# Kernel optimization log

Measured on AMD Instinct MI355X. Metric: run time of the kernel, lower is better.

The kernel has to match this reference:

```python
import jax, jax.numpy as jnp
import numpy as np

B, L, D = 4, 1024, 768
H, Dh = 12, 64
W_ONE_SIDED = 512


def setup_inputs() -> dict:
    key = jax.random.key(0)
    ks = jax.random.split(key, 14)
    std = 0.02
    def lin(k):
        return jax.random.normal(k, (D, D), jnp.float32) * std
    inp = {
        "hidden_states": jax.random.normal(ks[0], (B, L, D), jnp.float32),
        "Wq": lin(ks[1]), "bq": jnp.zeros((D,), jnp.float32),
        "Wk": lin(ks[2]), "bk": jnp.zeros((D,), jnp.float32),
        "Wv": lin(ks[3]), "bv": jnp.zeros((D,), jnp.float32),
        "Wqg": lin(ks[4]), "bqg": jnp.zeros((D,), jnp.float32),
        "Wkg": lin(ks[5]), "bkg": jnp.zeros((D,), jnp.float32),
        "Wvg": lin(ks[6]), "bvg": jnp.zeros((D,), jnp.float32),
    }
    pos = jnp.arange(L)
    # last 64 positions padded; first 8 tokens are global (CLS-like)
    inp["is_index_masked"] = jnp.broadcast_to(pos >= L - 64, (B, L))
    inp["is_index_global_attn"] = jnp.broadcast_to(pos < 8, (B, L))
    return inp


def _split_heads(x):
    # [B, L, D] -> [B, L, H, Dh]
    return x.reshape(B, L, H, Dh)


def reference(hidden_states, Wq, bq, Wk, bk, Wv, bv, Wqg, bqg, Wkg, bkg, Wvg, bvg,
              is_index_masked, is_index_global_attn):
    scale = 1.0 / np.sqrt(Dh)
    x = hidden_states
    Ql = _split_heads(x @ Wq + bq)
    Kl = _split_heads(x @ Wk + bk)
    Vl = _split_heads(x @ Wv + bv)
    Qg = _split_heads(x @ Wqg + bqg)
    Kg = _split_heads(x @ Wkg + bkg)
    Vg = _split_heads(x @ Wvg + bvg)

    neg_inf = jnp.finfo(x.dtype).min
    not_masked = ~is_index_masked
    not_global = ~is_index_global_attn

    # ---- local branch: doubled-K scores [B,H,L,2L] (first half: global-key
    # columns, second half: banded local-key columns), joint softmax ----
    s = jnp.einsum('bqhd,bkhd->bhqk', Ql, Kl) * scale  # [B,H,L,L]
    idx = jnp.arange(L)
    band = jnp.abs(idx[None, :] - idx[:, None]) <= W_ONE_SIDED  # [L,L]
    global_valid = (is_index_global_attn & not_masked)[:, None, None, :]      # [B,1,1,L]
    local_valid = (band[None, :, :] & (not_masked & not_global)[:, None, :])[:, None, :, :]  # [B,1,L,L]
    s_first = jnp.where(global_valid, s, neg_inf)
    s_second = jnp.where(local_valid, s, neg_inf)
    scores_local = jnp.concatenate([s_first, s_second], axis=-1)  # [B,H,L,2L]
    probs = jax.nn.softmax(scores_local.astype(jnp.float32), axis=-1).astype(x.dtype)
    probs = jnp.where(is_index_masked[:, None, :, None], 0.0, probs)
    # (p1 + p2) @ V  ==  p1 @ V + p2 @ V  since K/V are duplicated
    p_sum = probs[..., :L] + probs[..., L:]
    attn_local = jnp.einsum('bhqk,bkhd->bqhd', p_sum, Vl).reshape(B, L, D)

    # ---- global branch: full attention over global projections ----
    sg = jnp.einsum('bqhd,bkhd->bhqk', Qg, Kg) * scale
    sg = jnp.where(is_index_masked[:, None, None, :], neg_inf, sg)
    pg = jax.nn.softmax(sg.astype(jnp.float32), axis=-1).astype(x.dtype)
    pg = jnp.where(is_index_masked[:, None, :, None], 0.0, pg)
    attn_global = jnp.einsum('bhqk,bkhd->bqhd', pg, Vg).reshape(B, L, D)

    # ---- gated combine: global tokens take the global-attention output ----
    output = jnp.where(is_index_global_attn[:, :, None], attn_global, attn_local)
    return output
```

## Files before the change

### kernel.cpp

```cpp
#include <hip/hip_runtime.h>
#include <stdint.h>
#include <math.h>

#define LSEQ 1024
#define NB 4
#define DM 768
#define NHEAD 12
#define HD 64
#define LVALID 960
#define WIN 512

typedef unsigned short u16;
typedef __attribute__((ext_vector_type(8))) short s16x8;
typedef __attribute__((ext_vector_type(4))) float f32x4;

__device__ __forceinline__ u16 f2bf(float f) {
  union { float f; uint32_t u; } v; v.f = f;
  uint32_t r = v.u + 0x7fffu + ((v.u >> 16) & 1u);
  return (u16)(r >> 16);
}
__device__ __forceinline__ float bf2f(u16 h) {
  union { uint32_t u; float f; } v; v.u = ((uint32_t)h) << 16;
  return v.f;
}
__device__ __forceinline__ int swz8(int row, int chunk) {
  return row * 8 + (chunk ^ (row & 7));
}

__device__ __forceinline__ void gload_lds16(const void* g, void* l) {
  __builtin_amdgcn_global_load_lds(
      (const __attribute__((address_space(1))) unsigned int*)g,
      (__attribute__((address_space(3))) unsigned int*)l, 16, 0, 0);
}

#define BARW()                                  \
  do {                                          \
    asm volatile("" ::: "memory");              \
    __builtin_amdgcn_s_barrier();               \
    asm volatile("" ::: "memory");              \
  } while (0)
#define LGKM0() asm volatile("s_waitcnt lgkmcnt(0)" ::: "memory")
#define VMC4() asm volatile("s_waitcnt vmcnt(4)" ::: "memory")
#define VMC0() asm volatile("s_waitcnt vmcnt(0)" ::: "memory")

struct WPtrs { const float* w[6]; };
struct GemmPtrs { const u16* wt[6]; const float* bias[6]; u16* out[6]; };

__global__ __launch_bounds__(256) void prep(const float* __restrict__ x, u16* __restrict__ xb,
                                            WPtrs P, u16* __restrict__ wtb) {
  int bi = blockIdx.x;
  if (bi >= 864) {
    int i = ((bi - 864) * 256 + threadIdx.x) * 8;
    float4 a = *(const float4*)(x + i);
    float4 bq = *(const float4*)(x + i + 4);
    u16 t[8];
    t[0] = f2bf(a.x); t[1] = f2bf(a.y); t[2] = f2bf(a.z); t[3] = f2bf(a.w);
    t[4] = f2bf(bq.x); t[5] = f2bf(bq.y); t[6] = f2bf(bq.z); t[7] = f2bf(bq.w);
    *(uint4*)(xb + i) = *(uint4*)t;
    return;
  }
  int mat = bi / 144, rem = bi - mat * 144;
  int gx = rem % 12, gy = rem / 12;
  const float* W = P.w[mat];
  u16* Wt = wtb + (size_t)mat * DM * DM;
  __shared__ u16 tile[64][72];
  int k0 = gx * 64, n0 = gy * 64;
  int r4 = threadIdx.x >> 4;
  int c4 = (threadIdx.x & 15) * 4;
#pragma unroll
  for (int it = 0; it < 4; it++) {
    int r = it * 16 + r4;
    float4 v = *(const float4*)(W + (size_t)(k0 + r) * DM + n0 + c4);
    tile[c4 + 0][r] = f2bf(v.x);
    tile[c4 + 1][r] = f2bf(v.y);
    tile[c4 + 2][r] = f2bf(v.z);
    tile[c4 + 3][r] = f2bf(v.w);
  }
  __syncthreads();
  int rw = threadIdx.x >> 3, cw = (threadIdx.x & 7) * 8;
#pragma unroll
  for (int it = 0; it < 2; it++) {
    int r = it * 32 + rw;
    *(uint4*)(Wt + (size_t)(n0 + r) * DM + k0 + cw) = *(uint4*)&tile[r][cw];
  }
}

__global__ __launch_bounds__(512, 2) void gemm6(const u16* __restrict__ Xb, GemmPtrs P,
                                                u16* __restrict__ Vt) {
  int mat = blockIdx.z;
  int m0 = blockIdx.x * 256, n0 = blockIdx.y * 256;
  if (mat == 3 && (m0 & 1023) != 0) return;
  __shared__ __align__(16) u16 SMEM[65536];
  const u16* Wt = P.wt[mat];
  int tid = threadIdx.x;
  int w = tid >> 6, lane = tid & 63, qd = lane >> 4, l16 = lane & 15;
  int wm = w >> 2, wn = w & 3;
  int cx = l16 & 7;

  f32x4 acc[8][4];
  const f32x4 fz = {0.f, 0.f, 0.f, 0.f};
#pragma unroll
  for (int i = 0; i < 8; i++)
#pragma unroll
    for (int j = 0; j < 4; j++) acc[i][j] = fz;

  int aoff[2][2], boff[2][2];
#pragma unroll
  for (int j = 0; j < 2; j++) {
    int s = j * 512 + tid;
    int row = s >> 3;
    int col = ((s & 7) ^ (row & 7)) * 8;
#pragma unroll
    for (int h = 0; h < 2; h++) {
      aoff[j][h] = (m0 + h * 128 + row) * DM + col;
      boff[j][h] = (n0 + h * 128 + row) * DM + col;
    }
  }

  auto stageA = [&](int t, int h) {
#pragma unroll
    for (int j = 0; j < 2; j++)
      gload_lds16(Xb + (size_t)aoff[j][h] + t * 64,
                  &SMEM[(t & 1) * 32768 + h * 8192 + (j * 512 + w * 64) * 8]);
  };
  auto stageB = [&](int t, int h) {
#pragma unroll
    for (int j = 0; j < 2; j++)
      gload_lds16(Wt + (size_t)boff[j][h] + t * 64,
                  &SMEM[(t & 1) * 32768 + 16384 + h * 8192 + (j * 512 + w * 64) * 8]);
  };

  stageA(0, 0); stageA(0, 1);
  stageB(0, 0); stageB(0, 1);
  stageB(1, 0); stageB(1, 1);
  VMC4();
  BARW();

  const int rB = (wn & 1) * 64 + l16;

  auto tile = [&](int u) {
    const int buf = u & 1;
    const u16* Ab = &SMEM[buf * 32768 + wm * 8192];
    const u16* Bb = &SMEM[buf * 32768 + 16384 + (wn >> 1) * 8192];
    s16x8 af[4][2], bfr[4][2];
#pragma unroll
    for (int mi = 0; mi < 4; mi++)
#pragma unroll
      for (int ks = 0; ks < 2; ks++)
        af[mi][ks] = *(const s16x8*)(Ab + (mi * 16 + l16) * 64 + ((ks * 4 + qd) ^ cx) * 8);
#pragma unroll
    for (int ni = 0; ni < 2; ni++)
#pragma unroll
      for (int ks = 0; ks < 2; ks++)
        bfr[ni][ks] = *(const s16x8*)(Bb + (rB + ni * 16) * 64 + ((ks * 4 + qd) ^ cx) * 8);
    if (u < 11) stageA(u + 1, 0);
    BARW();
    LGKM0();
    __builtin_amdgcn_s_setprio(1);
#pragma unroll
    for (int mi = 0; mi < 4; mi++)
#pragma unroll
      for (int ni = 0; ni < 2; ni++)
#pragma unroll
        for (int ks = 0; ks < 2; ks++)
          acc[mi][ni] = __builtin_amdgcn_mfma_f32_16x16x32_bf16(af[mi][ks], bfr[ni][ks],
                                                                acc[mi][ni], 0, 0, 0);
    __builtin_amdgcn_s_setprio(0);
    BARW();
#pragma unroll
    for (int ni = 2; ni < 4; ni++)
#pragma unroll
      for (int ks = 0; ks < 2; ks++)
        bfr[ni][ks] = *(const s16x8*)(Bb + (rB + ni * 16) * 64 + ((ks * 4 + qd) ^ cx) * 8);
    if (u < 11) stageA(u + 1, 1);
    BARW();
    LGKM0();
    __builtin_amdgcn_s_setprio(1);
#pragma unroll
    for (int mi = 0; mi < 4; mi++)
#pragma unroll
      for (int ni = 2; ni < 4; ni++)
#pragma unroll
        for (int ks = 0; ks < 2; ks++)
          acc[mi][ni] = __builtin_amdgcn_mfma_f32_16x16x32_bf16(af[mi][ks], bfr[ni][ks],
                                                                acc[mi][ni], 0, 0, 0);
    __builtin_amdgcn_s_setprio(0);
    BARW();
#pragma unroll
    for (int mi = 0; mi < 4; mi++)
#pragma unroll
      for (int ks = 0; ks < 2; ks++)
        af[mi][ks] = *(const s16x8*)(Ab + ((mi + 4) * 16 + l16) * 64 + ((ks * 4 + qd) ^ cx) * 8);
    if (u < 10) stageB(u + 2, 0);
    BARW();
    LGKM0();
    __builtin_amdgcn_s_setprio(1);
#pragma unroll
    for (int mi = 0; mi < 4; mi++)
#pragma unroll
      for (int ni = 0; ni < 2; ni++)
#pragma unroll
        for (int ks = 0; ks < 2; ks++)
          acc[mi + 4][ni] = __builtin_amdgcn_mfma_f32_16x16x32_bf16(af[mi][ks], bfr[ni][ks],
                                                                    acc[mi + 4][ni], 0, 0, 0);
    __builtin_amdgcn_s_setprio(0);
    BARW();
    if (u < 10) {
      stageB(u + 2, 1);
      VMC4();
    } else {
      VMC0();
    }
    BARW();
    __builtin_amdgcn_s_setprio(1);
#pragma unroll
    for (int mi = 0; mi < 4; mi++)
#pragma unroll
      for (int ni = 2; ni < 4; ni++)
#pragma unroll
        for (int ks = 0; ks < 2; ks++)
          acc[mi + 4][ni] = __builtin_amdgcn_mfma_f32_16x16x32_bf16(af[mi][ks], bfr[ni][ks],
                                                                    acc[mi + 4][ni], 0, 0, 0);
    __builtin_amdgcn_s_setprio(0);
    BARW();
  };

  for (int u = 0; u < 12; ++u) tile(u);

  const float* bias = P.bias[mat];
  u16* outp = P.out[mat];
  int bb = m0 >> 10, t0 = m0 & 1023;
  __syncthreads();
  u16* Cs = &SMEM[0];
#pragma unroll
  for (int ni = 0; ni < 4; ni++) {
    int n = wn * 64 + ni * 16 + l16;
    float bvl = bias[n0 + n];
#pragma unroll
    for (int mi = 0; mi < 8; mi++) {
      int mb = wm * 128 + mi * 16 + qd * 4;
      u16 pk[4];
#pragma unroll
      for (int r = 0; r < 4; r++) {
        u16 v = f2bf(acc[mi][ni][r] + bvl);
        Cs[(mb + r) * 256 + n] = v;
        pk[r] = v;
      }
      if (mat == 2) {
        int gn = n0 + n, hh = gn >> 6, dd = gn & 63;
        *(uint2*)(Vt + ((size_t)(bb * NHEAD + hh) * HD + dd) * LSEQ + t0 + mb) =
            *(uint2*)pk;
      }
    }
  }
  __syncthreads();
#pragma unroll
  for (int it = 0; it < 16; it++) {
    int c = it * 512 + tid;
    int row = c >> 5, col = c & 31;
    *(uint4*)(outp + (size_t)(m0 + row) * DM + n0 + col * 8) = ((const uint4*)Cs)[c];
  }
}

__global__ __launch_bounds__(128) void attn_local(
    const u16* __restrict__ Qb, const u16* __restrict__ Kb,
    const u16* __restrict__ Vt, float* __restrict__ out) {
  int q0 = blockIdx.x * 32, h = blockIdx.y, b = blockIdx.z;
  __shared__ u16 Ks[64 * 64], Vs[64 * 64];
  __shared__ u16 Ps[2][16 * 64];
  int tid = threadIdx.x, w = tid >> 6, lane = tid & 63, qd = lane >> 4, l16 = lane & 15;

  int rowK[4], colK[4];
#pragma unroll
  for (int i = 0; i < 4; i++) {
    int s = (w * 4 + i) * 64 + lane;
    rowK[i] = s >> 3;
    colK[i] = ((s & 7) ^ (rowK[i] & 7)) * 8;
  }

  const u16* qrow = Qb + (size_t)(b * LSEQ + q0 + w * 16 + l16) * DM + h * HD;
  s16x8 af0 = *(const s16x8*)(qrow + qd * 8);
  s16x8 af1 = *(const s16x8*)(qrow + 32 + qd * 8);

  float l_part[4] = {0.f, 0.f, 0.f, 0.f};
  f32x4 aO[4];
  const f32x4 fz = {0.f, 0.f, 0.f, 0.f};
#pragma unroll
  for (int nt = 0; nt < 4; nt++) aO[nt] = fz;

  for (int c = 0; c < 16; c++) {
    int kb = c * 64;
    if (c > 0 && !(kb < LVALID && kb + 63 >= q0 - WIN && kb <= q0 + 31 + WIN)) continue;
    __syncthreads();
#pragma unroll
    for (int i = 0; i < 4; i++) {
      gload_lds16(Kb + (size_t)(b * LSEQ + kb + rowK[i]) * DM + h * HD + colK[i],
                  Ks + (size_t)(w * 4 + i) * 512);
      gload_lds16(Vt + (size_t)((b * NHEAD + h) * HD + rowK[i]) * LSEQ + kb + colK[i],
                  Vs + (size_t)(w * 4 + i) * 512);
    }
    __syncthreads();

    float p[4][4];
#pragma unroll
    for (int nt = 0; nt < 4; nt++) {
      s16x8 bk0 = *(const s16x8*)(Ks + swz8(nt * 16 + l16, qd) * 8);
      s16x8 bk1 = *(const s16x8*)(Ks + swz8(nt * 16 + l16, 4 + qd) * 8);
      f32x4 s = fz;
      s = __builtin_amdgcn_mfma_f32_16x16x32_bf16(af0, bk0, s, 0, 0, 0);
      s = __builtin_amdgcn_mfma_f32_16x16x32_bf16(af1, bk1, s, 0, 0, 0);
      int k = kb + nt * 16 + l16;
#pragma unroll
      for (int r = 0; r < 4; r++) {
        int q = q0 + w * 16 + qd * 4 + r;
        bool valid = (k < 8) || (k < LVALID && (k - q) <= WIN && (q - k) <= WIN);
        float sv = valid ? s[r] * 0.125f : -1e30f;
        p[nt][r] = __expf(sv);
        l_part[r] += p[nt][r];
      }
    }

#pragma unroll
    for (int nt = 0; nt < 4; nt++) {
      int chunk = nt * 2 + (l16 >> 3);
      int within = l16 & 7;
#pragma unroll
      for (int r = 0; r < 4; r++) {
        int qrow2 = qd * 4 + r;
        Ps[w][swz8(qrow2, chunk) * 8 + within] = f2bf(p[nt][r]);
      }
    }

    s16x8 pf0 = *(const s16x8*)(&Ps[w][0] + swz8(l16, qd) * 8);
    s16x8 pf1 = *(const s16x8*)(&Ps[w][0] + swz8(l16, 4 + qd) * 8);
#pragma unroll
    for (int nt = 0; nt < 4; nt++) {
      s16x8 v0 = *(const s16x8*)(Vs + swz8(nt * 16 + l16, qd) * 8);
      s16x8 v1 = *(const s16x8*)(Vs + swz8(nt * 16 + l16, 4 + qd) * 8);
      aO[nt] = __builtin_amdgcn_mfma_f32_16x16x32_bf16(pf0, v0, aO[nt], 0, 0, 0);
      aO[nt] = __builtin_amdgcn_mfma_f32_16x16x32_bf16(pf1, v1, aO[nt], 0, 0, 0);
    }
  }

#pragma unroll
  for (int off = 1; off < 16; off <<= 1)
#pragma unroll
    for (int r = 0; r < 4; r++) l_part[r] += __shfl_xor(l_part[r], off);
  float inv[4];
#pragma unroll
  for (int r = 0; r < 4; r++) inv[r] = 1.0f / l_part[r];
#pragma unroll
  for (int nt = 0; nt < 4; nt++)
#pragma unroll
    for (int r = 0; r < 4; r++) {
      int q = q0 + w * 16 + qd * 4 + r;
      out[(size_t)(b * LSEQ + q) * DM + h * HD + nt * 16 + l16] = aO[nt][r] * inv[r];
    }
}

__global__ __launch_bounds__(256) void attn_global(
    const u16* __restrict__ Qgb, const u16* __restrict__ Kgb,
    const u16* __restrict__ Vgb, float* __restrict__ out) {
  int h = blockIdx.x, b = blockIdx.y;
  __shared__ float p_lds[8][960];
  __shared__ float partial[4][8][64];
  int tid = threadIdx.x, w = tid >> 6, lane = tid & 63, qd = lane >> 4, l16 = lane & 15;

  {
    float4 z = {0.f, 0.f, 0.f, 0.f};
#pragma unroll
    for (int it = 0; it < 4; it++) {
      int idx = it * 256 + tid;
      int r = idx >> 4, cc = idx & 15;
      *(float4*)(out + (size_t)(b * LSEQ + LVALID + r) * DM + h * HD + cc * 4) = z;
    }
  }

  const u16* qbase = Qgb + (size_t)(b * LSEQ + l16) * DM + h * HD;
  s16x8 af0 = *(const s16x8*)(qbase + qd * 8);
  s16x8 af1 = *(const s16x8*)(qbase + 32 + qd * 8);
  const f32x4 fz = {0.f, 0.f, 0.f, 0.f};
#pragma unroll
  for (int t = 0; t < 15; t++) {
    int kb = (w + 4 * t) * 16;
    const u16* kbase = Kgb + (size_t)(b * LSEQ + kb + l16) * DM + h * HD;
    s16x8 bk0 = *(const s16x8*)(kbase + qd * 8);
    s16x8 bk1 = *(const s16x8*)(kbase + 32 + qd * 8);
    f32x4 s = fz;
    s = __builtin_amdgcn_mfma_f32_16x16x32_bf16(af0, bk0, s, 0, 0, 0);
    s = __builtin_amdgcn_mfma_f32_16x16x32_bf16(af1, bk1, s, 0, 0, 0);
    if (qd < 2) {
#pragma unroll
      for (int r = 0; r < 4; r++)
        p_lds[qd * 4 + r][kb + l16] = s[r] * 0.125f;
    }
  }
  __syncthreads();

#pragma unroll
  for (int qi = 0; qi < 2; qi++) {
    int q = w * 2 + qi;
    float m = -1e30f;
#pragma unroll
    for (int ki = 0; ki < 15; ki++) m = fmaxf(m, p_lds[q][ki * 64 + lane]);
#pragma unroll
    for (int off = 1; off < 64; off <<= 1) m = fmaxf(m, __shfl_xor(m, off));
    float e[15], ssum = 0.f;
#pragma unroll
    for (int ki = 0; ki < 15; ki++) {
      e[ki] = __expf(p_lds[q][ki * 64 + lane] - m);
      ssum += e[ki];
    }
#pragma unroll
    for (int off = 1; off < 64; off <<= 1) ssum += __shfl_xor(ssum, off);
    float inv = 1.0f / ssum;
#pragma unroll
    for (int ki = 0; ki < 15; ki++) p_lds[q][ki * 64 + lane] = e[ki] * inv;
  }
  __syncthreads();

  float acc[8] = {0.f, 0.f, 0.f, 0.f, 0.f, 0.f, 0.f, 0.f};
  const u16* vcol = Vgb + (size_t)b * LSEQ * DM + h * HD + lane;
  for (int kg = 0; kg < 60; kg++) {
    int k0 = w * 240 + kg * 4;
    float v0 = bf2f(vcol[(size_t)(k0 + 0) * DM]);
    float v1 = bf2f(vcol[(size_t)(k0 + 1) * DM]);
    float v2 = bf2f(vcol[(size_t)(k0 + 2) * DM]);
    float v3 = bf2f(vcol[(size_t)(k0 + 3) * DM]);
#pragma unroll
    for (int q = 0; q < 8; q++) {
      float4 p4 = *(const float4*)&p_lds[q][k0];
      acc[q] += p4.x * v0 + p4.y * v1 + p4.z * v2 + p4.w * v3;
    }
  }
#pragma unroll
  for (int q = 0; q < 8; q++) partial[w][q][lane] = acc[q];
  __syncthreads();
#pragma unroll
  for (int i = 0; i < 2; i++) {
    int idx = tid + 256 * i;
    int q = idx >> 6, d = idx & 63;
    float sum = partial[0][q][d] + partial[1][q][d] + partial[2][q][d] + partial[3][q][d];
    out[(size_t)(b * LSEQ + q) * DM + h * HD + d] = sum;
  }
}

extern "C" void kernel_launch(void* const* d_in, const int* in_sizes, int n_in,
                              void* d_out, int out_size, void* d_ws, size_t ws_size,
                              hipStream_t stream) {
  const float* x = (const float*)d_in[0];
  float* out = (float*)d_out;
  char* ws = (char*)d_ws;

  const size_t XB_SZ = (size_t)4096 * DM * 2;
  const size_t WT_SZ = (size_t)6 * DM * DM * 2;
  const size_t MAT_SZ = (size_t)4096 * DM;
  u16* Xb = (u16*)ws;
  u16* Wt = (u16*)(ws + XB_SZ);
  u16* QKV = (u16*)(ws + XB_SZ + WT_SZ);
  u16* Vt = (u16*)(ws + XB_SZ + WT_SZ + (size_t)6 * MAT_SZ * 2);

  u16* Ql = QKV + 0 * MAT_SZ;
  u16* Kl = QKV + 1 * MAT_SZ;
  u16* Vl = QKV + 2 * MAT_SZ;
  u16* Qg = QKV + 3 * MAT_SZ;
  u16* Kg = QKV + 4 * MAT_SZ;
  u16* Vg = QKV + 5 * MAT_SZ;

  WPtrs wp;
  wp.w[0] = (const float*)d_in[1];
  wp.w[1] = (const float*)d_in[3];
  wp.w[2] = (const float*)d_in[5];
  wp.w[3] = (const float*)d_in[7];
  wp.w[4] = (const float*)d_in[9];
  wp.w[5] = (const float*)d_in[11];
  prep<<<2400, 256, 0, stream>>>(x, Xb, wp, Wt);

  GemmPtrs gp;
  const int bidx[6] = {2, 4, 6, 8, 10, 12};
  u16* outs[6] = {Ql, Kl, Vl, Qg, Kg, Vg};
  for (int i = 0; i < 6; i++) {
    gp.wt[i] = Wt + (size_t)i * DM * DM;
    gp.bias[i] = (const float*)d_in[bidx[i]];
    gp.out[i] = outs[i];
  }
  gemm6<<<dim3(16, 3, 6), 512, 0, stream>>>(Xb, gp, Vt);

  attn_local<<<dim3(30, 12, 4), 128, 0, stream>>>(Ql, Kl, Vt, out);
  attn_global<<<dim3(12, 4), 256, 0, stream>>>(Qg, Kg, Vg, out);
}
```

Before: 201.2 us.

## Compact gemm grid with XCD-aware mapping, deepen A prefetch, read K/V directly in local attention

The projection GEMM launch drops its early-exiting blocks and maps a 1D grid of 252 blocks onto matrices and tiles so neighbouring work lands on the same XCD. The A-tile prefetch is moved one phase earlier, raising the outstanding-load wait count. Local attention drops its LDS staging of K and V along with both block barriers and loads MFMA operands straight from global memory, relying on the cache. It also remaps blocks so that each XCD handles contiguous (head, batch) groups. The trade-off is more uncoalesced global reads per wave in exchange for removing synchronisation.

```diff
diff --git a/kernel.cpp b/kernel.cpp
--- a/kernel.cpp
+++ b/kernel.cpp
@@ -40,7 +40,7 @@
     asm volatile("" ::: "memory");              \
   } while (0)
 #define LGKM0() asm volatile("s_waitcnt lgkmcnt(0)" ::: "memory")
-#define VMC4() asm volatile("s_waitcnt vmcnt(4)" ::: "memory")
+#define VMC6() asm volatile("s_waitcnt vmcnt(6)" ::: "memory")
 #define VMC0() asm volatile("s_waitcnt vmcnt(0)" ::: "memory")
 
 struct WPtrs { const float* w[6]; };
@@ -87,9 +87,23 @@
 
 __global__ __launch_bounds__(512, 2) void gemm6(const u16* __restrict__ Xb, GemmPtrs P,
                                                 u16* __restrict__ Vt) {
-  int mat = blockIdx.z;
-  int m0 = blockIdx.x * 256, n0 = blockIdx.y * 256;
-  if (mat == 3 && (m0 & 1023) != 0) return;
+  int lid = blockIdx.x;
+  int xcd = lid & 7, pos = lid >> 3;
+  int wid = (xcd < 4) ? xcd * 32 + pos : 128 + (xcd - 4) * 31 + pos;
+  int gid = wid >> 4, m = wid & 15;
+  int mat, x, y;
+  if (gid < 15) {
+    int mm = gid / 3;
+    mat = (mm < 3) ? mm : mm + 1;
+    y = gid - mm * 3;
+    x = m;
+  } else {
+    mat = 3;
+    x = (m / 3) * 4;
+    y = m - (m / 3) * 3;
+  }
+  int m0 = x * 256, n0 = y * 256;
+
   __shared__ __align__(16) u16 SMEM[65536];
   const u16* Wt = P.wt[mat];
   int tid = threadIdx.x;
@@ -133,7 +147,8 @@
   stageA(0, 0); stageA(0, 1);
   stageB(0, 0); stageB(0, 1);
   stageB(1, 0); stageB(1, 1);
-  VMC4();
+  stageA(1, 0);
+  VMC6();
   BARW();
 
   const int rB = (wn & 1) * 64 + l16;
@@ -153,7 +168,7 @@
 #pragma unroll
       for (int ks = 0; ks < 2; ks++)
         bfr[ni][ks] = *(const s16x8*)(Bb + (rB + ni * 16) * 64 + ((ks * 4 + qd) ^ cx) * 8);
-    if (u < 11) stageA(u + 1, 0);
+    if (u <= 10) stageA(u + 1, 1);
     BARW();
     LGKM0();
     __builtin_amdgcn_s_setprio(1);
@@ -172,7 +187,6 @@
 #pragma unroll
       for (int ks = 0; ks < 2; ks++)
         bfr[ni][ks] = *(const s16x8*)(Bb + (rB + ni * 16) * 64 + ((ks * 4 + qd) ^ cx) * 8);
-    if (u < 11) stageA(u + 1, 1);
     BARW();
     LGKM0();
     __builtin_amdgcn_s_setprio(1);
@@ -191,7 +205,7 @@
 #pragma unroll
       for (int ks = 0; ks < 2; ks++)
         af[mi][ks] = *(const s16x8*)(Ab + ((mi + 4) * 16 + l16) * 64 + ((ks * 4 + qd) ^ cx) * 8);
-    if (u < 10) stageB(u + 2, 0);
+    if (u <= 9) stageB(u + 2, 0);
     BARW();
     LGKM0();
     __builtin_amdgcn_s_setprio(1);
@@ -205,9 +219,10 @@
                                                                     acc[mi + 4][ni], 0, 0, 0);
     __builtin_amdgcn_s_setprio(0);
     BARW();
-    if (u < 10) {
+    if (u <= 9) {
       stageB(u + 2, 1);
-      VMC4();
+      stageA(u + 2, 0);
+      VMC6();
     } else {
       VMC0();
     }
@@ -265,23 +280,21 @@
 __global__ __launch_bounds__(128) void attn_local(
     const u16* __restrict__ Qb, const u16* __restrict__ Kb,
     const u16* __restrict__ Vt, float* __restrict__ out) {
-  int q0 = blockIdx.x * 32, h = blockIdx.y, b = blockIdx.z;
-  __shared__ u16 Ks[64 * 64], Vs[64 * 64];
+  int bid = blockIdx.x;
+  int wid = (bid & 7) * 180 + (bid >> 3);
+  int q0 = (wid % 30) * 32;
+  int hb = wid / 30;
+  int h = hb % NHEAD, b = hb / NHEAD;
   __shared__ u16 Ps[2][16 * 64];
   int tid = threadIdx.x, w = tid >> 6, lane = tid & 63, qd = lane >> 4, l16 = lane & 15;
-
-  int rowK[4], colK[4];
-#pragma unroll
-  for (int i = 0; i < 4; i++) {
-    int s = (w * 4 + i) * 64 + lane;
-    rowK[i] = s >> 3;
-    colK[i] = ((s & 7) ^ (rowK[i] & 7)) * 8;
-  }
 
   const u16* qrow = Qb + (size_t)(b * LSEQ + q0 + w * 16 + l16) * DM + h * HD;
   s16x8 af0 = *(const s16x8*)(qrow + qd * 8);
   s16x8 af1 = *(const s16x8*)(qrow + 32 + qd * 8);
 
+  const u16* kb_base = Kb + (size_t)(b * LSEQ) * DM + h * HD;
+  const u16* vt_base = Vt + (size_t)((b * NHEAD + h) * HD) * LSEQ;
+
   float l_part[4] = {0.f, 0.f, 0.f, 0.f};
   f32x4 aO[4];
   const f32x4 fz = {0.f, 0.f, 0.f, 0.f};
@@ -291,21 +304,13 @@
   for (int c = 0; c < 16; c++) {
     int kb = c * 64;
     if (c > 0 && !(kb < LVALID && kb + 63 >= q0 - WIN && kb <= q0 + 31 + WIN)) continue;
-    __syncthreads();
-#pragma unroll
-    for (int i = 0; i < 4; i++) {
-      gload_lds16(Kb + (size_t)(b * LSEQ + kb + rowK[i]) * DM + h * HD + colK[i],
-                  Ks + (size_t)(w * 4 + i) * 512);
-      gload_lds16(Vt + (size_t)((b * NHEAD + h) * HD + rowK[i]) * LSEQ + kb + colK[i],
-                  Vs + (size_t)(w * 4 + i) * 512);
-    }
-    __syncthreads();
 
     float p[4][4];
 #pragma unroll
     for (int nt = 0; nt < 4; nt++) {
-      s16x8 bk0 = *(const s16x8*)(Ks + swz8(nt * 16 + l16, qd) * 8);
-      s16x8 bk1 = *(const s16x8*)(Ks + swz8(nt * 16 + l16, 4 + qd) * 8);
+      const u16* krow = kb_base + (size_t)(kb + nt * 16 + l16) * DM;
+      s16x8 bk0 = *(const s16x8*)(krow + qd * 8);
+      s16x8 bk1 = *(const s16x8*)(krow + 32 + qd * 8);
       f32x4 s = fz;
       s = __builtin_amdgcn_mfma_f32_16x16x32_bf16(af0, bk0, s, 0, 0, 0);
       s = __builtin_amdgcn_mfma_f32_16x16x32_bf16(af1, bk1, s, 0, 0, 0);
@@ -335,8 +340,9 @@
     s16x8 pf1 = *(const s16x8*)(&Ps[w][0] + swz8(l16, 4 + qd) * 8);
 #pragma unroll
     for (int nt = 0; nt < 4; nt++) {
-      s16x8 v0 = *(const s16x8*)(Vs + swz8(nt * 16 + l16, qd) * 8);
-      s16x8 v1 = *(const s16x8*)(Vs + swz8(nt * 16 + l16, 4 + qd) * 8);
+      const u16* vrow = vt_base + (size_t)(nt * 16 + l16) * LSEQ + kb;
+      s16x8 v0 = *(const s16x8*)(vrow + qd * 8);
+      s16x8 v1 = *(const s16x8*)(vrow + 32 + qd * 8);
       aO[nt] = __builtin_amdgcn_mfma_f32_16x16x32_bf16(pf0, v0, aO[nt], 0, 0, 0);
       aO[nt] = __builtin_amdgcn_mfma_f32_16x16x32_bf16(pf1, v1, aO[nt], 0, 0, 0);
     }
@@ -484,8 +490,8 @@
     gp.bias[i] = (const float*)d_in[bidx[i]];
     gp.out[i] = outs[i];
   }
-  gemm6<<<dim3(16, 3, 6), 512, 0, stream>>>(Xb, gp, Vt);
-
-  attn_local<<<dim3(30, 12, 4), 128, 0, stream>>>(Ql, Kl, Vt, out);
+  gemm6<<<252, 512, 0, stream>>>(Xb, gp, Vt);
+
+  attn_local<<<1440, 128, 0, stream>>>(Ql, Kl, Vt, out);
   attn_global<<<dim3(12, 4), 256, 0, stream>>>(Qg, Kg, Vg, out);
 }
```

New measurement: 236.4 us. 1.18x slower.
